# Optimization experiments

Measured on AMD Instinct MI355X. Metric: run time of the kernel, lower is better.

The kernel has to match this reference:

```python
import jax, jax.numpy as jnp
import numpy as np

B, T, D, H, DH, PD = 4, 1024, 1024, 16, 64, 4
DFF = 4 * D
EPS = 1e-5

# Plucker pair index vectors for point_dim=4: pairs (0,1),(0,2),(0,3),(1,2),(1,3),(2,3)
_PI = jnp.array([0, 0, 0, 1, 1, 2])
_PJ = jnp.array([1, 2, 3, 2, 3, 3])
_J6 = jnp.array([[0,0,0,0,0,1],[0,0,0,0,-1,0],[0,0,0,1,0,0],
                 [0,0,1,0,0,0],[0,-1,0,0,0,0],[1,0,0,0,0,0]], dtype=jnp.float32)

def layer_norm(x, g, b):
    mu = jnp.mean(x, axis=-1, keepdims=True)
    var = jnp.var(x, axis=-1, keepdims=True)
    return (x - mu) * jax.lax.rsqrt(var + EPS) * g + b

def exterior(p1, p2):
    # p1,p2: [B,T,H,4] -> normalized Plucker line [B,T,H,6]
    L = p1[..., _PI] * p2[..., _PJ] - p1[..., _PJ] * p2[..., _PI]
    n = jnp.maximum(jnp.linalg.norm(L, axis=-1, keepdims=True), 1e-12)
    return L / n

def linear(x, w, b=None):
    y = jnp.einsum('...i,oi->...o', x, w)
    return y + b if b is not None else y


def setup_inputs() -> dict:
    key = jax.random.key(0)
    ks = jax.random.split(key, 16)
    s = 0.02
    return {
        'x': jax.random.normal(ks[0], (B, T, D), jnp.float32),
        'ln1_g': jnp.ones((D,), jnp.float32), 'ln1_b': jnp.zeros((D,), jnp.float32),
        'qkv_w': jax.random.normal(ks[1], (3 * D, D), jnp.float32) * s,
        'qkv_b': jnp.zeros((3 * D,), jnp.float32),
        'w1w': jax.random.normal(ks[2], (PD * H, D), jnp.float32) * s,
        'w2w': jax.random.normal(ks[3], (PD * H, D), jnp.float32) * s,
        'w1r': jax.random.normal(ks[4], (PD * H, D), jnp.float32) * s,
        'w2r': jax.random.normal(ks[5], (PD * H, D), jnp.float32) * s,
        'memv_w': jax.random.normal(ks[6], (D, D), jnp.float32) * s,
        'memv_b': jnp.zeros((D,), jnp.float32),
        'memg_w': jax.random.normal(ks[7], (H, D), jnp.float32) * s,
        'memg_b': jnp.zeros((H,), jnp.float32),
        'mem_scale': jnp.full((H,), 0.1, jnp.float32),
        'out_w': jax.random.normal(ks[8], (D, D), jnp.float32) * s,
        'out_b': jnp.zeros((D,), jnp.float32),
        'decay_logits': jnp.full((H,), 4.6, jnp.float32),
        'ln2_g': jnp.ones((D,), jnp.float32), 'ln2_b': jnp.zeros((D,), jnp.float32),
        'fc1_w': jax.random.normal(ks[9], (DFF, D), jnp.float32) * s,
        'fc1_b': jnp.zeros((DFF,), jnp.float32),
        'fc2_w': jax.random.normal(ks[10], (D, DFF), jnp.float32) * s,
        'fc2_b': jnp.zeros((D,), jnp.float32),
    }


def attn_forward(h, qkv_w, qkv_b, w1w, w2w, w1r, w2r, memv_w, memv_b,
                 memg_w, memg_b, mem_scale, out_w, out_b, decay_logits):
    # Standard causal attention (dropout = identity, eval mode)
    qkv = linear(h, qkv_w, qkv_b).reshape(B, T, 3, H, DH)
    q, k, v = [jnp.transpose(qkv[:, :, i], (0, 2, 1, 3)) for i in range(3)]  # [B,H,T,dh]
    scores = jnp.einsum('bhqd,bhkd->bhqk', q, k) * (DH ** -0.5)
    causal_mask = jnp.triu(jnp.ones((T, T), bool), k=1)
    scores = jnp.where(causal_mask, -jnp.inf, scores)
    attn = jax.nn.softmax(scores, axis=-1)
    seq_out = jnp.einsum('bhqk,bhkd->bhqd', attn, v).transpose(0, 2, 1, 3).reshape(B, T, D)

    # Geometric incidence memory branch
    x_prev = jnp.concatenate([jnp.zeros((B, 1, D), h.dtype), h[:, :-1]], axis=1)
    w1 = linear(x_prev, w1w).reshape(B, T, H, PD)
    w2 = linear(h, w2w).reshape(B, T, H, PD)
    write_lines = exterior(w1, w2)                   # [B,T,H,6]
    r1 = linear(h, w1r).reshape(B, T, H, PD)
    r2 = linear(h, w2r).reshape(B, T, H, PD)
    read_lines = exterior(r1, r2)                    # [B,T,H,6]
    J_write = jnp.einsum('bthi,ij->bthj', write_lines, _J6)
    incidence = jnp.einsum('bihp,bjhp->bhij', read_lines, J_write)  # [B,H,T,T]
    inc_abs = jnp.abs(incidence)

    # per-head exponential decay over strictly-past positions (i > j)
    decays = jax.nn.sigmoid(decay_logits)            # [H]
    pos = jnp.arange(T, dtype=h.dtype)
    diffs = pos[:, None] - pos[None, :]              # [T,T]
    past = diffs > 0
    # decays**diffs, masked to strictly-past (subsumes the causal masked_fill on inc_abs)
    weights = jnp.where(past, decays[:, None, None] ** jnp.maximum(diffs, 0.0), 0.0)  # [H,T,T]
    mem_score = jnp.einsum('bhij,hij->bhi', inc_abs, weights)  # [B,H,T]

    mem_val = linear(h, memv_w, memv_b)              # [B,T,D]
    gate = jax.nn.sigmoid(linear(h, memg_w, memg_b)) # [B,T,H]
    gated = jax.nn.sigmoid(mem_score.transpose(0, 2, 1) * mem_scale) * gate
    gated = jnp.mean(gated, axis=-1, keepdims=True)  # [B,T,1]
    return linear(seq_out + gated * mem_val, out_w, out_b)


def reference(x, ln1_g, ln1_b, qkv_w, qkv_b, w1w, w2w, w1r, w2r,
              memv_w, memv_b, memg_w, memg_b, mem_scale, out_w, out_b,
              decay_logits, ln2_g, ln2_b, fc1_w, fc1_b, fc2_w, fc2_b):
    # Pre-LN transformer block: x + Attn(LN(x)); x + MLP(LN(x))
    h = layer_norm(x, ln1_g, ln1_b)
    x = x + attn_forward(h, qkv_w, qkv_b, w1w, w2w, w1r, w2r, memv_w, memv_b,
                         memg_w, memg_b, mem_scale, out_w, out_b, decay_logits)
    h2 = layer_norm(x, ln2_g, ln2_b)
    mlp = linear(jax.nn.gelu(linear(h2, fc1_w, fc1_b), approximate=False), fc2_w, fc2_b)
    return x + mlp
```

## Files before the change

kernel.cpp:

```cpp
#include <hip/hip_runtime.h>
#include <math.h>

typedef __bf16 bf16;
typedef float f32x4 __attribute__((ext_vector_type(4)));
typedef bf16 bf16x8 __attribute__((ext_vector_type(8)));
typedef bf16 bf16x4 __attribute__((ext_vector_type(4)));

#define DEV __device__ __forceinline__

DEV void async16(const void* g, void* s) {
  __builtin_amdgcn_global_load_lds(
      (const __attribute__((address_space(1))) unsigned int*)g,
      (__attribute__((address_space(3))) unsigned int*)s, 16, 0, 0);
}

DEV f32x4 mfma16(bf16x8 a, bf16x8 b, f32x4 c) {
  return __builtin_amdgcn_mfma_f32_16x16x32_bf16(a, b, c, 0, 0, 0);
}

DEV float sigf(float x) { return 1.0f / (1.0f + __expf(-x)); }

__global__ __launch_bounds__(256)
void cast_w_k(const float* __restrict__ qkv_w, const float* __restrict__ w1w,
              const float* __restrict__ w2w, const float* __restrict__ w1r,
              const float* __restrict__ w2r, const float* __restrict__ memg_w,
              const float* __restrict__ memv_w, const float* __restrict__ out_w,
              const float* __restrict__ fc1_w, const float* __restrict__ fc2_w,
              bf16* __restrict__ dst)
{
  const long i = ((long)blockIdx.x * 256 + threadIdx.x) * 4;
  if (i >= 14024704L) return;
  float4 v;
  if      (i < 3145728L)  v = *(const float4*)&qkv_w[i];
  else if (i < 3211264L)  v = *(const float4*)&w1w[i - 3145728L];
  else if (i < 3276800L)  v = *(const float4*)&w2w[i - 3211264L];
  else if (i < 3342336L)  v = *(const float4*)&w1r[i - 3276800L];
  else if (i < 3407872L)  v = *(const float4*)&w2r[i - 3342336L];
  else if (i < 3424256L)  v = *(const float4*)&memg_w[i - 3407872L];
  else if (i < 3538944L)  v = make_float4(0.f, 0.f, 0.f, 0.f);
  else if (i < 4587520L)  v = *(const float4*)&memv_w[i - 3538944L];
  else if (i < 5636096L)  v = *(const float4*)&out_w[i - 4587520L];
  else if (i < 9830400L)  v = *(const float4*)&fc1_w[i - 5636096L];
  else                    v = *(const float4*)&fc2_w[i - 9830400L];
  bf16x4 y;
  y[0] = (bf16)v.x; y[1] = (bf16)v.y; y[2] = (bf16)v.z; y[3] = (bf16)v.w;
  *(bf16x4*)&dst[i] = y;
}

__global__ __launch_bounds__(256)
void ln_k(const float* __restrict__ x, const float* __restrict__ g,
          const float* __restrict__ bb, bf16* __restrict__ out)
{
  const int row = blockIdx.x, tid = threadIdx.x;
  const float4 xv = ((const float4*)(x + (long)row * 1024))[tid];
  float s  = xv.x + xv.y + xv.z + xv.w;
  float ss = xv.x * xv.x + xv.y * xv.y + xv.z * xv.z + xv.w * xv.w;
#pragma unroll
  for (int off = 1; off < 64; off <<= 1) {
    s  += __shfl_xor(s, off);
    ss += __shfl_xor(ss, off);
  }
  __shared__ float red[8];
  const int wave = tid >> 6, lane = tid & 63;
  if (lane == 0) { red[wave] = s; red[4 + wave] = ss; }
  __syncthreads();
  s  = red[0] + red[1] + red[2] + red[3];
  ss = red[4] + red[5] + red[6] + red[7];
  const float mu  = s * (1.0f / 1024.0f);
  const float var = ss * (1.0f / 1024.0f) - mu * mu;
  const float inv = rsqrtf(var + 1e-5f);
  const float4 gv = ((const float4*)g)[tid];
  const float4 bv = ((const float4*)bb)[tid];
  bf16x4 y;
  y[0] = (bf16)((xv.x - mu) * inv * gv.x + bv.x);
  y[1] = (bf16)((xv.y - mu) * inv * gv.y + bv.y);
  y[2] = (bf16)((xv.z - mu) * inv * gv.z + bv.z);
  y[3] = (bf16)((xv.w - mu) * inv * gv.w + bv.w);
  *(bf16x4*)&out[(long)row * 1024 + tid * 4] = y;
}

__global__ __launch_bounds__(256)
void ln2red_k(const float* __restrict__ part, const float* __restrict__ out_b,
              const float* __restrict__ x, const float* __restrict__ g,
              const float* __restrict__ bb, float* __restrict__ x2,
              bf16* __restrict__ h)
{
  const int row = blockIdx.x, tid = threadIdx.x;
  const long idx = (long)row * 1024 + tid * 4;
  const float4 p0 = *(const float4*)&part[idx];
  const float4 p1 = *(const float4*)&part[idx + 4194304];
  const float4 xr = *(const float4*)&x[idx];
  const float4 ob = *(const float4*)&out_b[tid * 4];
  float4 xv;
  xv.x = p0.x + p1.x + xr.x + ob.x;
  xv.y = p0.y + p1.y + xr.y + ob.y;
  xv.z = p0.z + p1.z + xr.z + ob.z;
  xv.w = p0.w + p1.w + xr.w + ob.w;
  *(float4*)&x2[idx] = xv;
  float s  = xv.x + xv.y + xv.z + xv.w;
  float ss = xv.x * xv.x + xv.y * xv.y + xv.z * xv.z + xv.w * xv.w;
#pragma unroll
  for (int off = 1; off < 64; off <<= 1) {
    s  += __shfl_xor(s, off);
    ss += __shfl_xor(ss, off);
  }
  __shared__ float red[8];
  const int wave = tid >> 6, lane = tid & 63;
  if (lane == 0) { red[wave] = s; red[4 + wave] = ss; }
  __syncthreads();
  s  = red[0] + red[1] + red[2] + red[3];
  ss = red[4] + red[5] + red[6] + red[7];
  const float mu  = s * (1.0f / 1024.0f);
  const float var = ss * (1.0f / 1024.0f) - mu * mu;
  const float inv = rsqrtf(var + 1e-5f);
  const float4 gv = ((const float4*)g)[tid];
  const float4 bv = ((const float4*)bb)[tid];
  bf16x4 y;
  y[0] = (bf16)((xv.x - mu) * inv * gv.x + bv.x);
  y[1] = (bf16)((xv.y - mu) * inv * gv.y + bv.y);
  y[2] = (bf16)((xv.z - mu) * inv * gv.z + bv.z);
  y[3] = (bf16)((xv.w - mu) * inv * gv.w + bv.w);
  *(bf16x4*)&h[idx] = y;
}

enum { M_BIAS_RES = 0, M_GELU = 1 };

#define GEMM_CORE(Aptr, Bptr, Kloop, Kstride)                                \
  __shared__ __align__(16) bf16 As[128 * 32];                                \
  __shared__ __align__(16) bf16 Bs[128 * 32];                                \
  const int tid = threadIdx.x;                                               \
  const int wave = tid >> 6, lane = tid & 63;                                \
  const int fr = lane & 15, fq = lane >> 4;                                  \
  const long bm = (long)blockIdx.y * 128;                                    \
  const long bn = (long)blockIdx.x * 128;                                    \
  const int wm = (wave >> 1) * 64, wn = (wave & 1) * 64;                     \
  const int sr = wave * 16 + (lane >> 2);                                    \
  const int sc = (lane & 3) * 8;                                             \
  const bf16* ag0 = Aptr + (bm + sr) * (long)Kstride + sc;                   \
  const bf16* ag1 = Aptr + (bm + 64 + sr) * (long)Kstride + sc;              \
  const bf16* bg0 = Bptr + (bn + sr) * (long)Kstride + sc;                   \
  const bf16* bg1 = Bptr + (bn + 64 + sr) * (long)Kstride + sc;              \
  bf16* as0 = &As[(wave * 16) * 32];                                         \
  bf16* as1 = &As[(64 + wave * 16) * 32];                                    \
  bf16* bs0 = &Bs[(wave * 16) * 32];                                         \
  bf16* bs1 = &Bs[(64 + wave * 16) * 32];                                    \
  f32x4 acc[4][4] = {};                                                      \
  for (int kt = 0; kt < Kloop; kt += 32) {                                   \
    __syncthreads();                                                         \
    async16(ag0 + kt, as0);                                                  \
    async16(ag1 + kt, as1);                                                  \
    async16(bg0 + kt, bs0);                                                  \
    async16(bg1 + kt, bs1);                                                  \
    __syncthreads();                                                         \
    bf16x8 af[4], bfr[4];                                                    \
    _Pragma("unroll")                                                        \
    for (int i = 0; i < 4; ++i)                                              \
      af[i] = *(const bf16x8*)&As[(wm + i * 16 + fr) * 32 + fq * 8];         \
    _Pragma("unroll")                                                        \
    for (int j = 0; j < 4; ++j)                                              \
      bfr[j] = *(const bf16x8*)&Bs[(wn + j * 16 + fr) * 32 + fq * 8];        \
    _Pragma("unroll")                                                        \
    for (int i = 0; i < 4; ++i)                                              \
      _Pragma("unroll")                                                      \
      for (int j = 0; j < 4; ++j)                                            \
        acc[i][j] = mfma16(af[i], bfr[j], acc[i][j]);                        \
  }

template <int MODE>
__global__ __launch_bounds__(256, 4)
void gemm_k(const bf16* __restrict__ A, const bf16* __restrict__ Bw,
            int N, int K,
            const float* __restrict__ bias, const float* __restrict__ res,
            float* __restrict__ outf, bf16* __restrict__ outb)
{
  GEMM_CORE(A, Bw, K, K)
#pragma unroll
  for (int i = 0; i < 4; ++i) {
    const long row0 = bm + wm + i * 16 + fq * 4;
#pragma unroll
    for (int j = 0; j < 4; ++j) {
      const long col = bn + wn + j * 16 + fr;
#pragma unroll
      for (int r = 0; r < 4; ++r) {
        const long rr = row0 + r;
        float v = acc[i][j][r];
        if (MODE == M_BIAS_RES) {
          outf[rr * N + col] = v + bias[col] + res[rr * N + col];
        } else {
          v += bias[col];
          v = 0.5f * v * (1.0f + erff(v * 0.70710678118654752f));
          outb[rr * N + col] = (bf16)v;
        }
      }
    }
  }
}

template <int KLEN, int KSTRIDE>
__global__ __launch_bounds__(256, 4)
void gemm_splitk_k(const bf16* __restrict__ A_, const bf16* __restrict__ Bw_,
                   float* __restrict__ part)
{
  const bf16* A  = A_  + (long)blockIdx.z * KLEN;
  const bf16* Bw = Bw_ + (long)blockIdx.z * KLEN;
  float* outf = part + (long)blockIdx.z * 4194304;
  GEMM_CORE(A, Bw, KLEN, KSTRIDE)
#pragma unroll
  for (int i = 0; i < 4; ++i) {
    const long row0 = bm + wm + i * 16 + fq * 4;
#pragma unroll
    for (int j = 0; j < 4; ++j) {
      const long col = bn + wn + j * 16 + fr;
#pragma unroll
      for (int r = 0; r < 4; ++r)
        outf[(row0 + r) * 1024 + col] = acc[i][j][r];
    }
  }
}

__global__ __launch_bounds__(256)
void fc2red_k(const float* __restrict__ part, const float* __restrict__ x2,
              const float* __restrict__ fc2_b, float* __restrict__ out)
{
  const long row = blockIdx.x;
  const int tid = threadIdx.x;
  const long idx = row * 1024 + tid * 4;
  const float4 p0 = *(const float4*)&part[idx];
  const float4 p1 = *(const float4*)&part[idx + 4194304];
  const float4 xv = *(const float4*)&x2[idx];
  const float4 bv = *(const float4*)&fc2_b[tid * 4];
  float4 o;
  o.x = p0.x + p1.x + xv.x + bv.x;
  o.y = p0.y + p1.y + xv.y + bv.y;
  o.z = p0.z + p1.z + xv.z + bv.z;
  o.w = p0.w + p1.w + xv.w + bv.w;
  *(float4*)&out[idx] = o;
}

__global__ __launch_bounds__(256, 4)
void gemm3_k(const bf16* __restrict__ A, const bf16* __restrict__ Bw,
             const float* __restrict__ qkv_b, const float* __restrict__ memv_b,
             bf16* __restrict__ qk_out ,
             bf16* __restrict__ vt_out ,
             float* __restrict__ w4out ,
             float* __restrict__ memval )
{
  GEMM_CORE(A, Bw, 1024, 1024)
  if (bn < 3072) {
#pragma unroll
    for (int i = 0; i < 4; ++i) {
      const long row0 = bm + wm + i * 16 + fq * 4;
      const long b = row0 >> 10, t0 = row0 & 1023;
#pragma unroll
      for (int j = 0; j < 4; ++j) {
        const long col = bn + wn + j * 16 + fr;
        const long i3 = col >> 10;
        const long hh = (col >> 6) & 15;
        const long d  = col & 63;
        const float bs = qkv_b[col];
        if (i3 == 2) {
          bf16x4 y;
#pragma unroll
          for (int r = 0; r < 4; ++r) y[r] = (bf16)(acc[i][j][r] + bs);
          *(bf16x4*)&vt_out[((b * 16 + hh) * 64 + d) * 1024 + t0] = y;
        } else {
          const float sc2 = (i3 == 0) ? 0.125f : 1.0f;
          const long base = i3 * 4194304 + ((b * 16 + hh) * 1024 + t0) * 64 + d;
#pragma unroll
          for (int r = 0; r < 4; ++r)
            qk_out[base + r * 64] = (bf16)((acc[i][j][r] + bs) * sc2);
        }
      }
    }
  } else if (bn < 3456) {
#pragma unroll
    for (int i = 0; i < 4; ++i) {
      const long row0 = bm + wm + i * 16 + fq * 4;
#pragma unroll
      for (int j = 0; j < 4; ++j) {
        const long col = bn + wn + j * 16 + fr - 3072;
#pragma unroll
        for (int r = 0; r < 4; ++r)
          w4out[(row0 + r) * 384 + col] = acc[i][j][r];
      }
    }
  } else {
#pragma unroll
    for (int i = 0; i < 4; ++i) {
      const long row0 = bm + wm + i * 16 + fq * 4;
#pragma unroll
      for (int j = 0; j < 4; ++j) {
        const long col = bn + wn + j * 16 + fr - 3456;
        const float bs = memv_b[col];
#pragma unroll
        for (int r = 0; r < 4; ++r)
          memval[(row0 + r) * 1024 + col] = acc[i][j][r] + bs;
      }
    }
  }
}

__global__ __launch_bounds__(256, 3)
void attn_k(const bf16* __restrict__ q, const bf16* __restrict__ k,
            const bf16* __restrict__ vt, const float* __restrict__ memval,
            const float* __restrict__ gbuf, bf16* __restrict__ comb)
{
  __shared__ __align__(16) bf16 Ks[64 * 72];
  __shared__ __align__(16) bf16 Vs[64 * 72];
  __shared__ __align__(16) bf16 Ps[4][16 * 72];
  const int bx = blockIdx.x, h = blockIdx.y, b = blockIdx.z;
  const int tid = threadIdx.x;
  const int wave = tid >> 6, lane = tid & 63;
  const int fr = lane & 15, fq = lane >> 4;
  const long bh  = ((long)b * 16 + h) * 1024;
  const long bhv = ((long)b * 16 + h) * 64;

  for (int pass = 0; pass < 2; ++pass) {
    const int qt = pass ? 15 - bx : bx;
    const int qbase = qt * 64;
    const bf16x8 aq0 = *(const bf16x8*)&q[(bh + qbase + wave * 16 + fr) * 64 + fq * 8];
    const bf16x8 aq1 = *(const bf16x8*)&q[(bh + qbase + wave * 16 + fr) * 64 + 32 + fq * 8];

    f32x4 o[4] = {};
    float m_r[4] = {-1e30f, -1e30f, -1e30f, -1e30f};
    float l_r[4] = {0.0f, 0.0f, 0.0f, 0.0f};

    for (int kt = 0; kt <= qt; ++kt) {
      const int kb = kt * 64;
      __syncthreads();
#pragma unroll
      for (int rep = 0; rep < 2; ++rep) {
        const int c = rep * 256 + tid;
        const int key = c >> 3, seg = c & 7;
        *(bf16x8*)&Ks[key * 72 + seg * 8] =
            *(const bf16x8*)&k[(bh + kb + key) * 64 + seg * 8];
      }
#pragma unroll
      for (int rep = 0; rep < 2; ++rep) {
        const int c = rep * 256 + tid;
        const int d = c >> 3, seg = c & 7;
        *(bf16x8*)&Vs[d * 72 + seg * 8] =
            *(const bf16x8*)&vt[(bhv + d) * 1024 + kb + seg * 8];
      }
      __syncthreads();

      f32x4 s[4];
#pragma unroll
      for (int j = 0; j < 4; ++j) {
        const bf16x8 b0 = *(const bf16x8*)&Ks[(j * 16 + fr) * 72 + fq * 8];
        const bf16x8 b1 = *(const bf16x8*)&Ks[(j * 16 + fr) * 72 + 32 + fq * 8];
        f32x4 tacc = {};
        tacc = mfma16(aq0, b0, tacc);
        tacc = mfma16(aq1, b1, tacc);
        s[j] = tacc;
      }
      if (kt == qt) {
#pragma unroll
        for (int j = 0; j < 4; ++j)
#pragma unroll
          for (int r = 0; r < 4; ++r)
            if (kb + j * 16 + fr > qbase + wave * 16 + fq * 4 + r) s[j][r] = -1e30f;
      }

      float alpha[4];
#pragma unroll
      for (int r = 0; r < 4; ++r) {
        float t = fmaxf(fmaxf(s[0][r], s[1][r]), fmaxf(s[2][r], s[3][r]));
#pragma unroll
        for (int off = 1; off < 16; off <<= 1) t = fmaxf(t, __shfl_xor(t, off));
        const float mn = fmaxf(m_r[r], t);
        alpha[r] = __expf(m_r[r] - mn);
        m_r[r] = mn;
        float ls = 0.0f;
#pragma unroll
        for (int j = 0; j < 4; ++j) {
          const float p = __expf(s[j][r] - mn);
          s[j][r] = p;
          ls += p;
        }
#pragma unroll
        for (int off = 1; off < 16; off <<= 1) ls += __shfl_xor(ls, off);
        l_r[r] = l_r[r] * alpha[r] + ls;
#pragma unroll
        for (int jd = 0; jd < 4; ++jd) o[jd][r] *= alpha[r];
      }

#pragma unroll
      for (int j = 0; j < 4; ++j)
#pragma unroll
        for (int r = 0; r < 4; ++r)
          Ps[wave][(fq * 4 + r) * 72 + j * 16 + fr] = (bf16)s[j][r];

      const bf16x8 ap0 = *(const bf16x8*)&Ps[wave][fr * 72 + fq * 8];
      const bf16x8 ap1 = *(const bf16x8*)&Ps[wave][fr * 72 + 32 + fq * 8];
#pragma unroll
      for (int jd = 0; jd < 4; ++jd) {
        const bf16x8 b0 = *(const bf16x8*)&Vs[(jd * 16 + fr) * 72 + fq * 8];
        const bf16x8 b1 = *(const bf16x8*)&Vs[(jd * 16 + fr) * 72 + 32 + fq * 8];
        o[jd] = mfma16(ap0, b0, o[jd]);
        o[jd] = mfma16(ap1, b1, o[jd]);
      }
    }

#pragma unroll
    for (int r = 0; r < 4; ++r) {
      const long t_ = qbase + wave * 16 + fq * 4 + r;
      const long row = (long)b * 1024 + t_;
      const float inv = 1.0f / l_r[r];
      const float gv = gbuf[row];
#pragma unroll
      for (int jd = 0; jd < 4; ++jd) {
        const long col = h * 64 + jd * 16 + fr;
        comb[row * 1024 + col] =
            (bf16)(o[jd][r] * inv + gv * memval[row * 1024 + col]);
      }
    }
  }
}

DEV void ext6(const float* p1, const float* p2, float* out) {
  const float L0 = p1[0] * p2[1] - p1[1] * p2[0];
  const float L1 = p1[0] * p2[2] - p1[2] * p2[0];
  const float L2 = p1[0] * p2[3] - p1[3] * p2[0];
  const float L3 = p1[1] * p2[2] - p1[2] * p2[1];
  const float L4 = p1[1] * p2[3] - p1[3] * p2[1];
  const float L5 = p1[2] * p2[3] - p1[3] * p2[2];
  const float nrm = sqrtf(L0*L0 + L1*L1 + L2*L2 + L3*L3 + L4*L4 + L5*L5);
  const float inv = 1.0f / fmaxf(nrm, 1e-12f);
  out[0] = L0 * inv; out[1] = L1 * inv; out[2] = L2 * inv;
  out[3] = L3 * inv; out[4] = L4 * inv; out[5] = L5 * inv;
}

__global__ __launch_bounds__(256)
void memscore_k(const float* __restrict__ w4o,
                const float* __restrict__ decay_logits, float* __restrict__ ms)
{
  __shared__ __align__(16) float jwS[256 * 8];
  const int IT[10] = {0,1,1,2,2,2,3,3,3,3};
  const int JC[10] = {0,0,1,0,1,2,0,1,2,3};
  const int it = IT[blockIdx.x], jc = JC[blockIdx.x];
  const int bh = blockIdx.y, hh = bh & 15, b = bh >> 4;
  const float d = sigf(decay_logits[hh]);
  const float invd = 1.0f / d;
  const int j0 = jc * 256;
  {
    const int j = j0 + threadIdx.x;
    const long nj = (long)b * 1024 + j;
    float p1[4], p2[4], wl[6];
    if (j == 0) { p1[0] = p1[1] = p1[2] = p1[3] = 0.0f; }
    else {
      const float* s = w4o + (nj - 1) * 384 + hh * 4;
      p1[0] = s[0]; p1[1] = s[1]; p1[2] = s[2]; p1[3] = s[3];
    }
    { const float* s = w4o + nj * 384 + 64 + hh * 4;
      p2[0] = s[0]; p2[1] = s[1]; p2[2] = s[2]; p2[3] = s[3]; }
    ext6(p1, p2, wl);
    float* dstS = &jwS[threadIdx.x * 8];
    dstS[0] =  wl[5]; dstS[1] = -wl[4]; dstS[2] =  wl[3];
    dstS[3] =  wl[2]; dstS[4] = -wl[1]; dstS[5] =  wl[0];
    dstS[6] = 0.0f;   dstS[7] = 0.0f;
  }
  __syncthreads();
  const int i = it * 256 + threadIdx.x;
  const long ni = (long)b * 1024 + i;
  float q1[4], q2[4], rv[6];
  { const float* s = w4o + ni * 384 + 128 + hh * 4;
    q1[0] = s[0]; q1[1] = s[1]; q1[2] = s[2]; q1[3] = s[3]; }
  { const float* s = w4o + ni * 384 + 192 + hh * 4;
    q2[0] = s[0]; q2[1] = s[1]; q2[2] = s[2]; q2[3] = s[3]; }
  ext6(q1, q2, rv);
  const int nj = (jc == it) ? (int)threadIdx.x : 256;
  float w = __expf(__logf(d) * (float)(i - j0));
  float s = 0.0f;
  for (int jj = 0; jj < nj; ++jj) {
    const float* row = &jwS[jj * 8];
    const float dot = rv[0] * row[0] + rv[1] * row[1] + rv[2] * row[2] +
                      rv[3] * row[3] + rv[4] * row[4] + rv[5] * row[5];
    s += fabsf(dot) * w;
    w *= invd;
  }
  atomicAdd(&ms[(long)bh * 1024 + i], s);
}

__global__ __launch_bounds__(256)
void gate_k(const float* __restrict__ w4o, const float* __restrict__ ms,
            const float* __restrict__ memg_b, const float* __restrict__ mem_scale,
            float* __restrict__ g)
{
  const int n = blockIdx.x * 256 + threadIdx.x;
  const int b = n >> 10, t = n & 1023;
  float acc = 0.0f;
#pragma unroll
  for (int h = 0; h < 16; ++h) {
    const float gate = sigf(w4o[(long)n * 384 + 256 + h] + memg_b[h]);
    acc += sigf(ms[((long)(b * 16 + h)) * 1024 + t] * mem_scale[h]) * gate;
  }
  g[n] = acc * (1.0f / 16.0f);
}

extern "C" void kernel_launch(void* const* d_in, const int* in_sizes, int n_in,
                              void* d_out, int out_size, void* d_ws, size_t ws_size,
                              hipStream_t stream) {
  (void)in_sizes; (void)n_in; (void)out_size; (void)ws_size;
  const float* x         = (const float*)d_in[0];
  const float* ln1_g     = (const float*)d_in[1];
  const float* ln1_b     = (const float*)d_in[2];
  const float* qkv_w     = (const float*)d_in[3];
  const float* qkv_b     = (const float*)d_in[4];
  const float* w1w       = (const float*)d_in[5];
  const float* w2w       = (const float*)d_in[6];
  const float* w1r       = (const float*)d_in[7];
  const float* w2r       = (const float*)d_in[8];
  const float* memv_w    = (const float*)d_in[9];
  const float* memv_b    = (const float*)d_in[10];
  const float* memg_w    = (const float*)d_in[11];
  const float* memg_b    = (const float*)d_in[12];
  const float* mem_scale = (const float*)d_in[13];
  const float* out_w     = (const float*)d_in[14];
  const float* out_b     = (const float*)d_in[15];
  const float* decay_l   = (const float*)d_in[16];
  const float* ln2_g     = (const float*)d_in[17];
  const float* ln2_b     = (const float*)d_in[18];
  const float* fc1_w     = (const float*)d_in[19];
  const float* fc1_b     = (const float*)d_in[20];
  const float* fc2_w     = (const float*)d_in[21];
  const float* fc2_b     = (const float*)d_in[22];

  char* ws = (char*)d_ws;
  bf16*  Wbf    = (bf16*)ws;
  bf16*  Wout   = Wbf + 4587520;
  bf16*  Wfc1   = Wbf + 5636096;
  bf16*  Wfc2   = Wbf + 9830400;
  bf16*  h_bf   = (bf16*)(ws + 28049408);
  bf16*  q_bf   = (bf16*)(ws + 36438016);
  bf16*  vt_bf  = q_bf + 2 * 4194304;
  float* oppart = (float*)(ws + 36438016);
  bf16*  fc1out = q_bf;
  float* w4out  = (float*)(ws + 78381056);
  float* msb    = (float*)(ws + 84672512);
  float* gbuf   = (float*)(ws + 84934656);
  float* memval = (float*)(ws + 88080384);
  float* fc2part = (float*)(ws + 69992448);
  bf16*  comb   = (bf16*)(ws + 104857600);
  float* x2     = (float*)(ws + 113246208);

  cast_w_k<<<13696, 256, 0, stream>>>(qkv_w, w1w, w2w, w1r, w2r, memg_w,
                                      memv_w, out_w, fc1_w, fc2_w, Wbf);
  ln_k<<<4096, 256, 0, stream>>>(x, ln1_g, ln1_b, h_bf);
  gemm3_k<<<dim3(35, 32), 256, 0, stream>>>(h_bf, Wbf, qkv_b, memv_b,
                                            q_bf, vt_bf, w4out, memval);
  hipMemsetAsync(msb, 0, 64 * 1024 * sizeof(float), stream);
  memscore_k<<<dim3(10, 64), 256, 0, stream>>>(w4out, decay_l, msb);
  gate_k<<<16, 256, 0, stream>>>(w4out, msb, memg_b, mem_scale, gbuf);
  attn_k<<<dim3(8, 16, 4), 256, 0, stream>>>(q_bf, q_bf + 4194304, vt_bf,
                                             memval, gbuf, comb);
  gemm_splitk_k<512, 1024><<<dim3(8, 32, 2), 256, 0, stream>>>(comb, Wout,
                                                               oppart);
  ln2red_k<<<4096, 256, 0, stream>>>(oppart, out_b, x, ln2_g, ln2_b, x2, h_bf);
  gemm_k<M_GELU><<<dim3(32, 32), 256, 0, stream>>>(h_bf, Wfc1, 4096, 1024,
                                                   fc1_b, nullptr, nullptr, fc1out);
  gemm_splitk_k<2048, 4096><<<dim3(8, 32, 2), 256, 0, stream>>>(fc1out, Wfc2,
                                                                fc2part);
  fc2red_k<<<4096, 256, 0, stream>>>(fc2part, x2, fc2_b, (float*)d_out);
}
```

Baseline: 433.3 us.

## Double-buffer GEMM LDS tiles to overlap async loads with MFMA compute

The shared GEMM core now keeps two LDS buffers for the A and B tiles. The first tile is loaded before the loop, and each iteration prefetches the next K tile with global_load_lds into the other buffer while MFMAs run on the current one. This drops one of the two barriers per iteration and hides global-load latency behind compute. In exchange, LDS per block doubles, and the GEMM kernels' launch bounds drop from 4 to 2 blocks per CU, which allows more registers but lowers occupancy.

After: 448.9 us. 1.04x slower.

```diff
diff --git a/kernel.cpp b/kernel.cpp
--- a/kernel.cpp
+++ b/kernel.cpp
@@ -126,8 +126,8 @@
 enum { M_BIAS_RES = 0, M_GELU = 1 };
 
 #define GEMM_CORE(Aptr, Bptr, Kloop, Kstride)                                \
-  __shared__ __align__(16) bf16 As[128 * 32];                                \
-  __shared__ __align__(16) bf16 Bs[128 * 32];                                \
+  __shared__ __align__(16) bf16 As[2][128 * 32];                             \
+  __shared__ __align__(16) bf16 Bs[2][128 * 32];                             \
   const int tid = threadIdx.x;                                               \
   const int wave = tid >> 6, lane = tid & 63;                                \
   const int fr = lane & 15, fq = lane >> 4;                                  \
@@ -140,25 +140,29 @@
   const bf16* ag1 = Aptr + (bm + 64 + sr) * (long)Kstride + sc;              \
   const bf16* bg0 = Bptr + (bn + sr) * (long)Kstride + sc;                   \
   const bf16* bg1 = Bptr + (bn + 64 + sr) * (long)Kstride + sc;              \
-  bf16* as0 = &As[(wave * 16) * 32];                                         \
-  bf16* as1 = &As[(64 + wave * 16) * 32];                                    \
-  bf16* bs0 = &Bs[(wave * 16) * 32];                                         \
-  bf16* bs1 = &Bs[(64 + wave * 16) * 32];                                    \
+  const int so0 = (wave * 16) * 32, so1 = (64 + wave * 16) * 32;             \
   f32x4 acc[4][4] = {};                                                      \
+  async16(ag0, &As[0][so0]);                                                 \
+  async16(ag1, &As[0][so1]);                                                 \
+  async16(bg0, &Bs[0][so0]);                                                 \
+  async16(bg1, &Bs[0][so1]);                                                 \
   for (int kt = 0; kt < Kloop; kt += 32) {                                   \
-    __syncthreads();                                                         \
-    async16(ag0 + kt, as0);                                                  \
-    async16(ag1 + kt, as1);                                                  \
-    async16(bg0 + kt, bs0);                                                  \
-    async16(bg1 + kt, bs1);                                                  \
-    __syncthreads();                                                         \
+    const int cur = (kt >> 5) & 1;                                           \
+    __syncthreads();         \
+    if (kt + 32 < Kloop) {                                                   \
+      const int nxt = cur ^ 1;                                               \
+      async16(ag0 + kt + 32, &As[nxt][so0]);                                 \
+      async16(ag1 + kt + 32, &As[nxt][so1]);                                 \
+      async16(bg0 + kt + 32, &Bs[nxt][so0]);                                 \
+      async16(bg1 + kt + 32, &Bs[nxt][so1]);                                 \
+    }                                                                        \
     bf16x8 af[4], bfr[4];                                                    \
     _Pragma("unroll")                                                        \
     for (int i = 0; i < 4; ++i)                                              \
-      af[i] = *(const bf16x8*)&As[(wm + i * 16 + fr) * 32 + fq * 8];         \
+      af[i] = *(const bf16x8*)&As[cur][(wm + i * 16 + fr) * 32 + fq * 8];    \
     _Pragma("unroll")                                                        \
     for (int j = 0; j < 4; ++j)                                              \
-      bfr[j] = *(const bf16x8*)&Bs[(wn + j * 16 + fr) * 32 + fq * 8];        \
+      bfr[j] = *(const bf16x8*)&Bs[cur][(wn + j * 16 + fr) * 32 + fq * 8];   \
     _Pragma("unroll")                                                        \
     for (int i = 0; i < 4; ++i)                                              \
       _Pragma("unroll")                                                      \
@@ -167,7 +171,7 @@
   }
 
 template <int MODE>
-__global__ __launch_bounds__(256, 4)
+__global__ __launch_bounds__(256, 2)
 void gemm_k(const bf16* __restrict__ A, const bf16* __restrict__ Bw,
             int N, int K,
             const float* __restrict__ bias, const float* __restrict__ res,
@@ -197,7 +201,7 @@
 }
 
 template <int KLEN, int KSTRIDE>
-__global__ __launch_bounds__(256, 4)
+__global__ __launch_bounds__(256, 2)
 void gemm_splitk_k(const bf16* __restrict__ A_, const bf16* __restrict__ Bw_,
                    float* __restrict__ part)
 {
@@ -237,7 +241,7 @@
   *(float4*)&out[idx] = o;
 }
 
-__global__ __launch_bounds__(256, 4)
+__global__ __launch_bounds__(256, 2)
 void gemm3_k(const bf16* __restrict__ A, const bf16* __restrict__ Bw,
              const float* __restrict__ qkv_b, const float* __restrict__ memv_b,
              bf16* __restrict__ qk_out ,
```

## Replace LDS-staged GEMM tiles with direct register loads and prefetch

Applied to the files above, without the earlier changes.

The shared GEMM core no longer stages A/B tiles through LDS with async global-to-LDS copies and two barriers per k-step. Each wave now loads its MFMA fragments directly from global memory into registers and prefetches the next k-slice while issuing MFMAs on the current one. Occupancy hints are dropped from launch bounds and K becomes a template parameter for gemm_k. This removes LDS traffic and synchronisation, but tile data is no longer shared between waves, so each A/B element is loaded twice from global or L2, and register pressure rises.

Measured after the change: 698.4 us. 61.2% more time.

```diff
diff --git a/kernel.cpp b/kernel.cpp
--- a/kernel.cpp
+++ b/kernel.cpp
@@ -7,12 +7,6 @@
 typedef bf16 bf16x4 __attribute__((ext_vector_type(4)));
 
 #define DEV __device__ __forceinline__
-
-DEV void async16(const void* g, void* s) {
-  __builtin_amdgcn_global_load_lds(
-      (const __attribute__((address_space(1))) unsigned int*)g,
-      (__attribute__((address_space(3))) unsigned int*)s, 16, 0, 0);
-}
 
 DEV f32x4 mfma16(bf16x8 a, bf16x8 b, f32x4 c) {
   return __builtin_amdgcn_mfma_f32_16x16x32_bf16(a, b, c, 0, 0, 0);
@@ -126,50 +120,42 @@
 enum { M_BIAS_RES = 0, M_GELU = 1 };
 
 #define GEMM_CORE(Aptr, Bptr, Kloop, Kstride)                                \
-  __shared__ __align__(16) bf16 As[128 * 32];                                \
-  __shared__ __align__(16) bf16 Bs[128 * 32];                                \
   const int tid = threadIdx.x;                                               \
   const int wave = tid >> 6, lane = tid & 63;                                \
   const int fr = lane & 15, fq = lane >> 4;                                  \
   const long bm = (long)blockIdx.y * 128;                                    \
   const long bn = (long)blockIdx.x * 128;                                    \
   const int wm = (wave >> 1) * 64, wn = (wave & 1) * 64;                     \
-  const int sr = wave * 16 + (lane >> 2);                                    \
-  const int sc = (lane & 3) * 8;                                             \
-  const bf16* ag0 = Aptr + (bm + sr) * (long)Kstride + sc;                   \
-  const bf16* ag1 = Aptr + (bm + 64 + sr) * (long)Kstride + sc;              \
-  const bf16* bg0 = Bptr + (bn + sr) * (long)Kstride + sc;                   \
-  const bf16* bg1 = Bptr + (bn + 64 + sr) * (long)Kstride + sc;              \
-  bf16* as0 = &As[(wave * 16) * 32];                                         \
-  bf16* as1 = &As[(64 + wave * 16) * 32];                                    \
-  bf16* bs0 = &Bs[(wave * 16) * 32];                                         \
-  bf16* bs1 = &Bs[(64 + wave * 16) * 32];                                    \
+  const bf16* aP = Aptr + (bm + wm + fr) * (long)Kstride + fq * 8;           \
+  const bf16* bP = Bptr + (bn + wn + fr) * (long)Kstride + fq * 8;           \
   f32x4 acc[4][4] = {};                                                      \
+  bf16x8 af0[4], bf0[4];                                                     \
+  _Pragma("unroll")                                                          \
+  for (int i = 0; i < 4; ++i) {                                              \
+    af0[i] = *(const bf16x8*)(aP + (long)i * 16 * Kstride);                  \
+    bf0[i] = *(const bf16x8*)(bP + (long)i * 16 * Kstride);                  \
+  }                                                                          \
   for (int kt = 0; kt < Kloop; kt += 32) {                                   \
-    __syncthreads();                                                         \
-    async16(ag0 + kt, as0);                                                  \
-    async16(ag1 + kt, as1);                                                  \
-    async16(bg0 + kt, bs0);                                                  \
-    async16(bg1 + kt, bs1);                                                  \
-    __syncthreads();                                                         \
-    bf16x8 af[4], bfr[4];                                                    \
+    const int knx = (kt + 32 < Kloop) ? kt + 32 : kt;       \
+    bf16x8 af1[4], bf1[4];                                                   \
     _Pragma("unroll")                                                        \
-    for (int i = 0; i < 4; ++i)                                              \
-      af[i] = *(const bf16x8*)&As[(wm + i * 16 + fr) * 32 + fq * 8];         \
-    _Pragma("unroll")                                                        \
-    for (int j = 0; j < 4; ++j)                                              \
-      bfr[j] = *(const bf16x8*)&Bs[(wn + j * 16 + fr) * 32 + fq * 8];        \
+    for (int i = 0; i < 4; ++i) {                                            \
+      af1[i] = *(const bf16x8*)(aP + (long)i * 16 * Kstride + knx);          \
+      bf1[i] = *(const bf16x8*)(bP + (long)i * 16 * Kstride + knx);          \
+    }                                                                        \
     _Pragma("unroll")                                                        \
     for (int i = 0; i < 4; ++i)                                              \
       _Pragma("unroll")                                                      \
       for (int j = 0; j < 4; ++j)                                            \
-        acc[i][j] = mfma16(af[i], bfr[j], acc[i][j]);                        \
-  }
-
-template <int MODE>
-__global__ __launch_bounds__(256, 4)
+        acc[i][j] = mfma16(af0[i], bf0[j], acc[i][j]);                       \
+    _Pragma("unroll")                                                        \
+    for (int i = 0; i < 4; ++i) { af0[i] = af1[i]; bf0[i] = bf1[i]; }        \
+  }
+
+template <int MODE, int K>
+__global__ __launch_bounds__(256)
 void gemm_k(const bf16* __restrict__ A, const bf16* __restrict__ Bw,
-            int N, int K,
+            int N,
             const float* __restrict__ bias, const float* __restrict__ res,
             float* __restrict__ outf, bf16* __restrict__ outb)
 {
@@ -197,7 +183,7 @@
 }
 
 template <int KLEN, int KSTRIDE>
-__global__ __launch_bounds__(256, 4)
+__global__ __launch_bounds__(256)
 void gemm_splitk_k(const bf16* __restrict__ A_, const bf16* __restrict__ Bw_,
                    float* __restrict__ part)
 {
@@ -237,7 +223,7 @@
   *(float4*)&out[idx] = o;
 }
 
-__global__ __launch_bounds__(256, 4)
+__global__ __launch_bounds__(256)
 void gemm3_k(const bf16* __restrict__ A, const bf16* __restrict__ Bw,
              const float* __restrict__ qkv_b, const float* __restrict__ memv_b,
              bf16* __restrict__ qk_out ,
@@ -557,7 +543,7 @@
   gemm_splitk_k<512, 1024><<<dim3(8, 32, 2), 256, 0, stream>>>(comb, Wout,
                                                                oppart);
   ln2red_k<<<4096, 256, 0, stream>>>(oppart, out_b, x, ln2_g, ln2_b, x2, h_bf);
-  gemm_k<M_GELU><<<dim3(32, 32), 256, 0, stream>>>(h_bf, Wfc1, 4096, 1024,
+  gemm_k<M_GELU, 1024><<<dim3(32, 32), 256, 0, stream>>>(h_bf, Wfc1, 4096,
                                                    fc1_b, nullptr, nullptr, fc1out);
   gemm_splitk_k<2048, 4096><<<dim3(8, 32, 2), 256, 0, stream>>>(fc1out, Wfc2,
                                                                 fc2part);
```
